# Performance work log

Hardware: AMD Instinct MI355X
Metric: run time of the kernel (lower is better)

Reference implementation:

```python
import jax, jax.numpy as jnp
import numpy as np

N_NODES = 100000
N_EDGES = 1600000
IN_DIM = 75
H_COMP = 64
H_BOND = 16
DEPTH = 3


def setup_inputs() -> dict:
    key = jax.random.key(0)
    ks = jax.random.split(key, 8)
    x = jax.random.normal(ks[0], (N_NODES, IN_DIM), dtype=jnp.float32)
    edge_index = jax.random.randint(ks[1], (2, N_EDGES), 0, N_NODES, dtype=jnp.int64)
    edge_attr = jax.random.normal(ks[2], (N_EDGES, H_BOND), dtype=jnp.float32)
    proj_w = jax.random.normal(ks[3], (IN_DIM, H_COMP), dtype=jnp.float32) * (1.0 / np.sqrt(IN_DIM))
    proj_b = jnp.zeros((H_COMP,), dtype=jnp.float32)
    u2_w = jax.random.normal(ks[4], (DEPTH, H_COMP + H_BOND, H_COMP), dtype=jnp.float32) * (1.0 / np.sqrt(H_COMP + H_BOND))
    u2_b = jnp.zeros((DEPTH, H_COMP), dtype=jnp.float32)
    u1_w = jax.random.normal(ks[5], (DEPTH, 2 * H_COMP, H_COMP), dtype=jnp.float32) * (1.0 / np.sqrt(2 * H_COMP))
    u1_b = jnp.zeros((DEPTH, H_COMP), dtype=jnp.float32)
    return {"x": x, "edge_index": edge_index, "edge_attr": edge_attr,
            "proj_w": proj_w, "proj_b": proj_b,
            "u2_w": u2_w, "u2_b": u2_b, "u1_w": u1_w, "u1_b": u1_b}


def reference(x, edge_index, edge_attr, proj_w, proj_b, u2_w, u2_b, u1_w, u1_b):
    # PyG default flow source_to_target: messages gathered from edge_index[0],
    # scatter-added at edge_index[1].
    src, dst = edge_index[0], edge_index[1]
    n = x.shape[0]
    # input projection: [N, in_dim] -> [N, H]
    h = x @ proj_w + proj_b
    for l in range(u2_w.shape[0]):
        # message: concat(x_j, edge_attr) -> Linear -> LeakyReLU(0.1)   [E, H+B] -> [E, H]
        z = jnp.concatenate([h[src], edge_attr], axis=-1)
        m = jax.nn.leaky_relu(z @ u2_w[l] + u2_b[l], negative_slope=0.1)
        # aggregate: scatter-add over destination nodes  [E, H] -> [N, H]
        agg = jax.ops.segment_sum(m, dst, num_segments=n)
        # update: concat(x, agg) -> Linear  [N, 2H] -> [N, H]
        h = jnp.concatenate([h, agg], axis=-1) @ u1_w[l] + u1_b[l]
    return h
```

## Files before the change

### kernel.cpp

```cpp
#include <hip/hip_runtime.h>

typedef __attribute__((ext_vector_type(8))) short frag_ab;
typedef __attribute__((ext_vector_type(4))) float frag_cd;
typedef __attribute__((ext_vector_type(4))) short short4v;

__device__ __forceinline__ short f2bf(float f) {
  union { float f; unsigned u; } v; v.f = f;
  unsigned r = v.u + 0x7fffu + ((v.u >> 16) & 1u);
  return (short)(r >> 16);
}

__global__ void wconv(const float* __restrict__ W, short* __restrict__ out,
                      int Keff, int S, int nmat)
{
  int tid = blockIdx.x * 256 + threadIdx.x;
  int per = S * 4 * 64;
  if (tid >= nmat * per) return;
  int m = tid / per, r = tid % per;
  int s = r / 256, ct = (r >> 6) & 3, ln = r & 63;
  const float* Wm = W + (size_t)m * Keff * 64;
  __align__(16) short tmp[8];
  for (int j = 0; j < 8; ++j) {
    int k = s * 32 + (ln >> 4) * 8 + j;
    int n = ct * 16 + (ln & 15);
    tmp[j] = (k < Keff) ? f2bf(Wm[k * 64 + n]) : (short)0;
  }
  *(uint4*)&out[((size_t)m * per + (size_t)(s * 4 + ct) * 64 + ln) * 8] = *(uint4*)tmp;
}

#define AS1 104
__global__ __launch_bounds__(256, 4) void proj_kernel(
    const float* __restrict__ x, const short* __restrict__ wt,
    const float* __restrict__ bias, short* __restrict__ hbf, int N)
{
  __shared__ __align__(16) short A[128 * AS1];
  int t = threadIdx.x;
  int nb = blockIdx.x * 128;
  int ln = t & 63;
  frag_ab bf[12];
  for (int s = 0; s < 3; ++s)
    for (int ct = 0; ct < 4; ++ct)
      bf[s * 4 + ct] = *(const frag_ab*)&wt[((size_t)(s * 4 + ct) * 64 + ln) * 8];
  for (int i = 0; i < 48; ++i) {
    int q = i * 256 + t; int el = q / 96; int c = q - el * 96;
    int rg = nb + el;
    float v = (c < 75 && rg < N) ? x[rg * 75 + c] : 0.f;
    A[el * AS1 + c] = f2bf(v);
  }
  __syncthreads();
  int wv = t >> 6;
  int lrow = ln & 15, lk = ln >> 4;
  frag_cd acc[2][4];
  for (int rt = 0; rt < 2; ++rt) for (int ct = 0; ct < 4; ++ct) {
    frag_cd z = {0.f, 0.f, 0.f, 0.f}; acc[rt][ct] = z;
  }
  for (int s = 0; s < 3; ++s) {
    frag_ab a0 = *(const frag_ab*)&A[(wv*32 + lrow) * AS1 + s*32 + lk*8];
    frag_ab a1 = *(const frag_ab*)&A[(wv*32 + 16 + lrow) * AS1 + s*32 + lk*8];
    for (int ct = 0; ct < 4; ++ct) {
      acc[0][ct] = __builtin_amdgcn_mfma_f32_16x16x32_bf16(a0, bf[s*4+ct], acc[0][ct], 0, 0, 0);
      acc[1][ct] = __builtin_amdgcn_mfma_f32_16x16x32_bf16(a1, bf[s*4+ct], acc[1][ct], 0, 0, 0);
    }
  }
  float bv[4];
  for (int ct = 0; ct < 4; ++ct) bv[ct] = bias[ct*16 + lrow];
  for (int rt = 0; rt < 2; ++rt)
    for (int ct = 0; ct < 4; ++ct)
      for (int r = 0; r < 4; ++r) {
        int row = wv*32 + rt*16 + lk*4 + r;
        int rg = nb + row;
        if (rg < N) hbf[(size_t)rg * 64 + ct*16 + lrow] = f2bf(acc[rt][ct][r] + bv[ct]);
      }
}

__global__ __launch_bounds__(256) void hist_kernel(
    const int* __restrict__ dst, int* __restrict__ counts, int E)
{
  int i = blockIdx.x * 256 + threadIdx.x;
  if (i < E) atomicAdd(&counts[dst[i]], 1);
}

#define SCAN_TILE 2048
__global__ __launch_bounds__(256) void scan_k1(
    const int* __restrict__ counts, int* __restrict__ offsets,
    int* __restrict__ bsum, int n)
{
  __shared__ int ts[256];
  int t = threadIdx.x;
  int base = blockIdx.x * SCAN_TILE + t * 8;
  int v[8]; int s = 0;
  for (int j = 0; j < 8; ++j) { v[j] = (base + j < n) ? counts[base + j] : 0; s += v[j]; }
  ts[t] = s; __syncthreads();
  for (int off = 1; off < 256; off <<= 1) {
    int x = (t >= off) ? ts[t - off] : 0;
    __syncthreads();
    ts[t] += x;
    __syncthreads();
  }
  if (t == 255) bsum[blockIdx.x] = ts[255];
  int run = (t > 0) ? ts[t - 1] : 0;
  for (int j = 0; j < 8; ++j) { if (base + j < n) offsets[base + j] = run; run += v[j]; }
}

__global__ void scan_k2(int* bsum, int nb) {
  if (threadIdx.x == 0 && blockIdx.x == 0) {
    int run = 0;
    for (int b = 0; b < nb; ++b) { int x = bsum[b]; bsum[b] = run; run += x; }
  }
}

__global__ __launch_bounds__(256) void scan_k3(
    int* __restrict__ offsets, const int* __restrict__ bsum, int n)
{
  int add = bsum[blockIdx.x];
  int base = blockIdx.x * SCAN_TILE + threadIdx.x;
  for (int j = 0; j < 8; ++j) { int i = base + j * 256; if (i < n) offsets[i] += add; }
}

__global__ __launch_bounds__(256) void scatter_kernel(
    const int* __restrict__ src, const int* __restrict__ dst,
    const float* __restrict__ attr, int* __restrict__ offsets,
    int2* __restrict__ sd, short* __restrict__ attr_s, int E)
{
  int e = blockIdx.x * 256 + threadIdx.x;
  if (e < E) {
    int d = dst[e];
    int p = atomicAdd(&offsets[d], 1);
    sd[p] = make_int2(src[e], d);
    const float4* a4 = (const float4*)(attr + (size_t)e * 16);
    float4 v0 = a4[0], v1 = a4[1], v2 = a4[2], v3 = a4[3];
    __align__(16) short tmp[16];
    tmp[0]=f2bf(v0.x); tmp[1]=f2bf(v0.y); tmp[2]=f2bf(v0.z); tmp[3]=f2bf(v0.w);
    tmp[4]=f2bf(v1.x); tmp[5]=f2bf(v1.y); tmp[6]=f2bf(v1.z); tmp[7]=f2bf(v1.w);
    tmp[8]=f2bf(v2.x); tmp[9]=f2bf(v2.y); tmp[10]=f2bf(v2.z); tmp[11]=f2bf(v2.w);
    tmp[12]=f2bf(v3.x); tmp[13]=f2bf(v3.y); tmp[14]=f2bf(v3.z); tmp[15]=f2bf(v3.w);
    *(uint4*)&attr_s[(size_t)p * 16]     = *(uint4*)&tmp[0];
    *(uint4*)&attr_s[(size_t)p * 16 + 8] = *(uint4*)&tmp[8];
  }
}

#define MS 66
__global__ __launch_bounds__(256, 4) void msg_kernel(
    const short* __restrict__ hbf, const short* __restrict__ attr_s,
    const int2* __restrict__ sd, const short* __restrict__ wt,
    const float* __restrict__ bias, float* __restrict__ agg, int E)
{
  __shared__ __align__(16) char u[128 * MS * 4];
  __shared__ int dstl[128];
  short* A = (short*)u;
  float* M = (float*)u;

  int t = threadIdx.x;
  int eb = blockIdx.x * 128;
  int ln = t & 63;

  if (t < 128) dstl[t] = (eb + t < E) ? sd[eb + t].y : -1;

  frag_ab bf[12];
  for (int s = 0; s < 3; ++s)
    for (int ct = 0; ct < 4; ++ct)
      bf[s * 4 + ct] = *(const frag_ab*)&wt[((size_t)(s * 4 + ct) * 64 + ln) * 8];

  for (int i = 0; i < 4; ++i) {
    int q = i * 256 + t; int el = q >> 3; int c = q & 7;
    int p = eb + el;
    int s = (p < E) ? sd[p].x : 0;
    *(uint4*)&A[el * AS1 + c * 8] = *(const uint4*)&hbf[(size_t)s * 64 + c * 8];
  }
  {
    int el = t >> 1, c = t & 1;
    int p = eb + el;
    uint4 v = {0u, 0u, 0u, 0u};
    if (p < E) v = *(const uint4*)&attr_s[(size_t)p * 16 + c * 8];
    *(uint4*)&A[el * AS1 + 64 + c * 8] = v;
    uint4 z = {0u, 0u, 0u, 0u};
    *(uint4*)&A[el * AS1 + 80 + c * 8] = z;
  }
  __syncthreads();

  int wv = t >> 6;
  int lrow = ln & 15, lk = ln >> 4;
  frag_cd acc[2][4];
  for (int rt = 0; rt < 2; ++rt) for (int ct = 0; ct < 4; ++ct) {
    frag_cd z = {0.f, 0.f, 0.f, 0.f}; acc[rt][ct] = z;
  }
  for (int s = 0; s < 3; ++s) {
    frag_ab a0 = *(const frag_ab*)&A[(wv*32 + lrow) * AS1 + s*32 + lk*8];
    frag_ab a1 = *(const frag_ab*)&A[(wv*32 + 16 + lrow) * AS1 + s*32 + lk*8];
    for (int ct = 0; ct < 4; ++ct) {
      acc[0][ct] = __builtin_amdgcn_mfma_f32_16x16x32_bf16(a0, bf[s*4+ct], acc[0][ct], 0, 0, 0);
      acc[1][ct] = __builtin_amdgcn_mfma_f32_16x16x32_bf16(a1, bf[s*4+ct], acc[1][ct], 0, 0, 0);
    }
  }
  float bv[4];
  for (int ct = 0; ct < 4; ++ct) bv[ct] = bias[ct*16 + lrow];

  __syncthreads();
  for (int rt = 0; rt < 2; ++rt)
    for (int ct = 0; ct < 4; ++ct)
      for (int r = 0; r < 4; ++r) {
        int row = wv*32 + rt*16 + lk*4 + r;
        float m = acc[rt][ct][r] + bv[ct];
        m = m > 0.f ? m : 0.1f * m;
        M[row * MS + ct*16 + lrow] = m;
      }
  __syncthreads();

  {
    int lo = wv * 32;
    bool end = false;
    if (ln < 32) {
      int di = dstl[lo + ln];
      end = (ln == 31) || (di != dstl[lo + ln + 1]);
    }
    unsigned long long bm = __ballot(end);
    unsigned em = (unsigned)bm;
    unsigned cm = em & ~(em & (0u - em)) & 0x7fffffffu;

    float s = 0.f;
#pragma unroll
    for (int i = 0; i < 32; ++i) {
      s += M[(lo + i) * MS + ln];
      if ((em >> i) & 1u) {
        int d = __builtin_amdgcn_readfirstlane(dstl[lo + i]);
        if (d >= 0) {
          float* dest = &agg[(size_t)d * 64 + ln];
          if ((cm >> i) & 1u) *dest = s;
          else unsafeAtomicAdd(dest, s);
        }
        s = 0.f;
      }
    }
  }
}

#define AS2 136
__global__ __launch_bounds__(256, 4) void upd_kernel(
    const short* __restrict__ hbf, float* __restrict__ agg,
    const short* __restrict__ wt, const float* __restrict__ bias,
    float* __restrict__ hout, short* __restrict__ hbfo, int N, int last)
{
  __shared__ __align__(16) short A[128 * AS2];
  int t = threadIdx.x;
  int nb = blockIdx.x * 128;
  int ln = t & 63;
  for (int i = 0; i < 4; ++i) {
    int q = i * 256 + t; int el = q >> 3; int c = q & 7;
    int rg = nb + el;
    uint4 v = {0u, 0u, 0u, 0u};
    if (rg < N) v = *(const uint4*)&hbf[(size_t)rg * 64 + c * 8];
    *(uint4*)&A[el * AS2 + c * 8] = v;
  }
  for (int i = 0; i < 8; ++i) {
    int q = i * 256 + t; int el = q >> 4; int c = q & 15;
    int rg = nb + el;
    float4 v = make_float4(0.f, 0.f, 0.f, 0.f);
    if (rg < N) {
      v = *(const float4*)&agg[(size_t)rg * 64 + c * 4];
      if (!last) {
        float4 z = make_float4(0.f, 0.f, 0.f, 0.f);
        *(float4*)&agg[(size_t)rg * 64 + c * 4] = z;
      }
    }
    short4v s4 = { f2bf(v.x), f2bf(v.y), f2bf(v.z), f2bf(v.w) };
    *(short4v*)&A[el * AS2 + 64 + c * 4] = s4;
  }
  __syncthreads();
  int wv = t >> 6;
  int lrow = ln & 15, lk = ln >> 4;
  frag_cd acc[2][4];
  for (int rt = 0; rt < 2; ++rt) for (int ct = 0; ct < 4; ++ct) {
    frag_cd z = {0.f, 0.f, 0.f, 0.f}; acc[rt][ct] = z;
  }
  for (int s = 0; s < 4; ++s) {
    frag_ab a0 = *(const frag_ab*)&A[(wv*32 + lrow) * AS2 + s*32 + lk*8];
    frag_ab a1 = *(const frag_ab*)&A[(wv*32 + 16 + lrow) * AS2 + s*32 + lk*8];
    for (int ct = 0; ct < 4; ++ct) {
      frag_ab b = *(const frag_ab*)&wt[((size_t)(s * 4 + ct) * 64 + ln) * 8];
      acc[0][ct] = __builtin_amdgcn_mfma_f32_16x16x32_bf16(a0, b, acc[0][ct], 0, 0, 0);
      acc[1][ct] = __builtin_amdgcn_mfma_f32_16x16x32_bf16(a1, b, acc[1][ct], 0, 0, 0);
    }
  }
  float bv[4];
  for (int ct = 0; ct < 4; ++ct) bv[ct] = bias[ct*16 + lrow];
  for (int rt = 0; rt < 2; ++rt)
    for (int ct = 0; ct < 4; ++ct)
      for (int r = 0; r < 4; ++r) {
        int row = wv*32 + rt*16 + lk*4 + r;
        int rg = nb + row;
        if (rg < N) {
          float v = acc[rt][ct][r] + bv[ct];
          if (last) hout[(size_t)rg * 64 + ct*16 + lrow] = v;
          hbfo[(size_t)rg * 64 + ct*16 + lrow] = f2bf(v);
        }
      }
}

extern "C" void kernel_launch(void* const* d_in, const int* in_sizes, int n_in,
                              void* d_out, int out_size, void* d_ws, size_t ws_size,
                              hipStream_t stream) {
  const float* x    = (const float*)d_in[0];
  const int*   ei   = (const int*)d_in[1];
  const float* attr = (const float*)d_in[2];
  const float* pw   = (const float*)d_in[3];
  const float* pb   = (const float*)d_in[4];
  const float* u2w  = (const float*)d_in[5];
  const float* u2b  = (const float*)d_in[6];
  const float* u1w  = (const float*)d_in[7];
  const float* u1b  = (const float*)d_in[8];

  const int N = in_sizes[0] / 75;
  const int E = in_sizes[1] / 2;
  const int* src = ei;
  const int* dst = ei + E;

  float* hout = (float*)d_out;
  char*  ws   = (char*)d_ws;
  size_t nh   = (size_t)N * 64;
  size_t off  = 0;
  short* hbf   = (short*)(ws + off); off += nh * 2;
  float* agg   = (float*)(ws + off); off += nh * 4;
  int2*  sd    = (int2*) (ws + off); off += (size_t)E * 8;
  short* attr_s= (short*)(ws + off); off += (size_t)E * 32;
  short* projt = (short*)(ws + off); off += 3 * 4 * 64 * 8 * 2;
  short* u2t   = (short*)(ws + off); off += (size_t)3 * 3 * 4 * 64 * 8 * 2;
  short* u1t   = (short*)(ws + off); off += (size_t)3 * 4 * 4 * 64 * 8 * 2;
  int* counts  = (int*)agg;
  int* offsets = counts + N;
  int* bsum    = offsets + N;

  const int NB = (N + 127) / 128;
  const int EB = (E + 127) / 128;
  const int GE = (E + 255) / 256;
  const int NS = (N + SCAN_TILE - 1) / SCAN_TILE;

  wconv<<<3, 256, 0, stream>>>(pw, projt, 75, 3, 1);
  wconv<<<9, 256, 0, stream>>>(u2w, u2t, 80, 3, 3);
  wconv<<<12, 256, 0, stream>>>(u1w, u1t, 128, 4, 3);
  proj_kernel<<<NB, 256, 0, stream>>>(x, projt, pb, hbf, N);
  hipMemsetAsync(counts, 0, (size_t)N * 4, stream);
  hist_kernel<<<GE, 256, 0, stream>>>(dst, counts, E);
  scan_k1<<<NS, 256, 0, stream>>>(counts, offsets, bsum, N);
  scan_k2<<<1, 64, 0, stream>>>(bsum, NS);
  scan_k3<<<NS, 256, 0, stream>>>(offsets, bsum, N);
  scatter_kernel<<<GE, 256, 0, stream>>>(src, dst, attr, offsets, sd, attr_s, E);

  hipMemsetAsync(agg, 0, nh * 4, stream);
  for (int l = 0; l < 3; ++l) {
    msg_kernel<<<EB, 256, 0, stream>>>(hbf, attr_s, sd,
                                       u2t + (size_t)l * 6144, u2b + l * 64,
                                       agg, E);
    upd_kernel<<<NB, 256, 0, stream>>>(hbf, agg,
                                       u1t + (size_t)l * 8192, u1b + l * 64,
                                       hout, hbf, N, l == 2);
  }
}
```

Baseline: 703.3 us.

## Load MFMA operands directly from global, drop LDS staging; precompute CSR ranks

The message and update kernels now load A-operand fragments straight from global memory into registers in MFMA layout instead of staging tiles through shared memory, which removes a barrier and LDS traffic. The message kernel also reloads weight fragments per step instead of keeping 12 in registers. The histogram kernel records each edge's rank so the scatter uses offset plus rank without a second atomic pass, and the block-sum scan becomes a wavefront shuffle scan. The trade-off is less coalesced global gathers (16-byte pieces per lane) and an extra per-edge rank array. The scan_k2 rewrite assumes at most 64 blocks.

New measurement: 695.9 us. Within noise of the previous version (-1.0%).

```diff
diff --git a/kernel.cpp b/kernel.cpp
--- a/kernel.cpp
+++ b/kernel.cpp
@@ -2,7 +2,6 @@
 
 typedef __attribute__((ext_vector_type(8))) short frag_ab;
 typedef __attribute__((ext_vector_type(4))) float frag_cd;
-typedef __attribute__((ext_vector_type(4))) short short4v;
 
 __device__ __forceinline__ short f2bf(float f) {
   union { float f; unsigned u; } v; v.f = f;
@@ -74,10 +73,11 @@
 }
 
 __global__ __launch_bounds__(256) void hist_kernel(
-    const int* __restrict__ dst, int* __restrict__ counts, int E)
+    const int* __restrict__ dst, int* __restrict__ counts,
+    int* __restrict__ rank, int E)
 {
   int i = blockIdx.x * 256 + threadIdx.x;
-  if (i < E) atomicAdd(&counts[dst[i]], 1);
+  if (i < E) rank[i] = atomicAdd(&counts[dst[i]], 1);
 }
 
 #define SCAN_TILE 2048
@@ -103,10 +103,14 @@
 }
 
 __global__ void scan_k2(int* bsum, int nb) {
-  if (threadIdx.x == 0 && blockIdx.x == 0) {
-    int run = 0;
-    for (int b = 0; b < nb; ++b) { int x = bsum[b]; bsum[b] = run; run += x; }
-  }
+  int ln = threadIdx.x;
+  int v = (ln < nb) ? bsum[ln] : 0;
+  int x = v;
+  for (int off = 1; off < 64; off <<= 1) {
+    int y = __shfl_up(x, off);
+    if (ln >= off) x += y;
+  }
+  if (ln < nb) bsum[ln] = x - v;
 }
 
 __global__ __launch_bounds__(256) void scan_k3(
@@ -119,13 +123,14 @@
 
 __global__ __launch_bounds__(256) void scatter_kernel(
     const int* __restrict__ src, const int* __restrict__ dst,
-    const float* __restrict__ attr, int* __restrict__ offsets,
-    int2* __restrict__ sd, short* __restrict__ attr_s, int E)
+    const float* __restrict__ attr, const int* __restrict__ offsets,
+    const int* __restrict__ rank, int2* __restrict__ sd,
+    short* __restrict__ attr_s, int E)
 {
   int e = blockIdx.x * 256 + threadIdx.x;
   if (e < E) {
     int d = dst[e];
-    int p = atomicAdd(&offsets[d], 1);
+    int p = offsets[d] + rank[e];
     sd[p] = make_int2(src[e], d);
     const float4* a4 = (const float4*)(attr + (size_t)e * 16);
     float4 v0 = a4[0], v1 = a4[1], v2 = a4[2], v3 = a4[3];
@@ -145,57 +150,42 @@
     const int2* __restrict__ sd, const short* __restrict__ wt,
     const float* __restrict__ bias, float* __restrict__ agg, int E)
 {
-  __shared__ __align__(16) char u[128 * MS * 4];
+  __shared__ float M[128 * MS];
   __shared__ int dstl[128];
-  short* A = (short*)u;
-  float* M = (float*)u;
-
   int t = threadIdx.x;
   int eb = blockIdx.x * 128;
   int ln = t & 63;
-
-  if (t < 128) dstl[t] = (eb + t < E) ? sd[eb + t].y : -1;
-
-  frag_ab bf[12];
-  for (int s = 0; s < 3; ++s)
-    for (int ct = 0; ct < 4; ++ct)
-      bf[s * 4 + ct] = *(const frag_ab*)&wt[((size_t)(s * 4 + ct) * 64 + ln) * 8];
-
-  for (int i = 0; i < 4; ++i) {
-    int q = i * 256 + t; int el = q >> 3; int c = q & 7;
-    int p = eb + el;
-    int s = (p < E) ? sd[p].x : 0;
-    *(uint4*)&A[el * AS1 + c * 8] = *(const uint4*)&hbf[(size_t)s * 64 + c * 8];
-  }
-  {
-    int el = t >> 1, c = t & 1;
-    int p = eb + el;
-    uint4 v = {0u, 0u, 0u, 0u};
-    if (p < E) v = *(const uint4*)&attr_s[(size_t)p * 16 + c * 8];
-    *(uint4*)&A[el * AS1 + 64 + c * 8] = v;
-    uint4 z = {0u, 0u, 0u, 0u};
-    *(uint4*)&A[el * AS1 + 80 + c * 8] = z;
-  }
-  __syncthreads();
-
   int wv = t >> 6;
   int lrow = ln & 15, lk = ln >> 4;
+
+  if (t < 128) dstl[t] = (eb + t < E) ? sd[eb + t].y : -1;
+
+  int p0 = eb + wv*32 + lrow;  if (p0 > E - 1) p0 = E - 1;
+  int p1 = p0 + 16;            if (p1 > E - 1) p1 = E - 1;
+  int s0 = sd[p0].x, s1 = sd[p1].x;
+
+  frag_ab a[3][2];
+  a[0][0] = *(const frag_ab*)&hbf[(size_t)s0 * 64 + lk*8];
+  a[0][1] = *(const frag_ab*)&hbf[(size_t)s1 * 64 + lk*8];
+  a[1][0] = *(const frag_ab*)&hbf[(size_t)s0 * 64 + 32 + lk*8];
+  a[1][1] = *(const frag_ab*)&hbf[(size_t)s1 * 64 + 32 + lk*8];
+  frag_ab z8 = {0,0,0,0,0,0,0,0};
+  a[2][0] = (lk < 2) ? *(const frag_ab*)&attr_s[(size_t)p0 * 16 + lk*8] : z8;
+  a[2][1] = (lk < 2) ? *(const frag_ab*)&attr_s[(size_t)p1 * 16 + lk*8] : z8;
+
   frag_cd acc[2][4];
   for (int rt = 0; rt < 2; ++rt) for (int ct = 0; ct < 4; ++ct) {
     frag_cd z = {0.f, 0.f, 0.f, 0.f}; acc[rt][ct] = z;
   }
-  for (int s = 0; s < 3; ++s) {
-    frag_ab a0 = *(const frag_ab*)&A[(wv*32 + lrow) * AS1 + s*32 + lk*8];
-    frag_ab a1 = *(const frag_ab*)&A[(wv*32 + 16 + lrow) * AS1 + s*32 + lk*8];
+  for (int s = 0; s < 3; ++s)
     for (int ct = 0; ct < 4; ++ct) {
-      acc[0][ct] = __builtin_amdgcn_mfma_f32_16x16x32_bf16(a0, bf[s*4+ct], acc[0][ct], 0, 0, 0);
-      acc[1][ct] = __builtin_amdgcn_mfma_f32_16x16x32_bf16(a1, bf[s*4+ct], acc[1][ct], 0, 0, 0);
-    }
-  }
+      frag_ab b = *(const frag_ab*)&wt[((size_t)(s * 4 + ct) * 64 + ln) * 8];
+      acc[0][ct] = __builtin_amdgcn_mfma_f32_16x16x32_bf16(a[s][0], b, acc[0][ct], 0, 0, 0);
+      acc[1][ct] = __builtin_amdgcn_mfma_f32_16x16x32_bf16(a[s][1], b, acc[1][ct], 0, 0, 0);
+    }
   float bv[4];
   for (int ct = 0; ct < 4; ++ct) bv[ct] = bias[ct*16 + lrow];
 
-  __syncthreads();
   for (int rt = 0; rt < 2; ++rt)
     for (int ct = 0; ct < 4; ++ct)
       for (int r = 0; r < 4; ++r) {
@@ -234,53 +224,55 @@
   }
 }
 
-#define AS2 136
 __global__ __launch_bounds__(256, 4) void upd_kernel(
     const short* __restrict__ hbf, float* __restrict__ agg,
     const short* __restrict__ wt, const float* __restrict__ bias,
     float* __restrict__ hout, short* __restrict__ hbfo, int N, int last)
 {
-  __shared__ __align__(16) short A[128 * AS2];
   int t = threadIdx.x;
   int nb = blockIdx.x * 128;
   int ln = t & 63;
-  for (int i = 0; i < 4; ++i) {
-    int q = i * 256 + t; int el = q >> 3; int c = q & 7;
-    int rg = nb + el;
-    uint4 v = {0u, 0u, 0u, 0u};
-    if (rg < N) v = *(const uint4*)&hbf[(size_t)rg * 64 + c * 8];
-    *(uint4*)&A[el * AS2 + c * 8] = v;
-  }
-  for (int i = 0; i < 8; ++i) {
-    int q = i * 256 + t; int el = q >> 4; int c = q & 15;
-    int rg = nb + el;
-    float4 v = make_float4(0.f, 0.f, 0.f, 0.f);
-    if (rg < N) {
-      v = *(const float4*)&agg[(size_t)rg * 64 + c * 4];
-      if (!last) {
-        float4 z = make_float4(0.f, 0.f, 0.f, 0.f);
-        *(float4*)&agg[(size_t)rg * 64 + c * 4] = z;
-      }
-    }
-    short4v s4 = { f2bf(v.x), f2bf(v.y), f2bf(v.z), f2bf(v.w) };
-    *(short4v*)&A[el * AS2 + 64 + c * 4] = s4;
-  }
-  __syncthreads();
   int wv = t >> 6;
   int lrow = ln & 15, lk = ln >> 4;
+  int r0 = nb + wv*32 + lrow;
+  int r1 = r0 + 16;
+
+  frag_ab z8 = {0,0,0,0,0,0,0,0};
+  frag_ab a[4][2];
+  a[0][0] = (r0 < N) ? *(const frag_ab*)&hbf[(size_t)r0 * 64 + lk*8]      : z8;
+  a[0][1] = (r1 < N) ? *(const frag_ab*)&hbf[(size_t)r1 * 64 + lk*8]      : z8;
+  a[1][0] = (r0 < N) ? *(const frag_ab*)&hbf[(size_t)r0 * 64 + 32 + lk*8] : z8;
+  a[1][1] = (r1 < N) ? *(const frag_ab*)&hbf[(size_t)r1 * 64 + 32 + lk*8] : z8;
+  for (int si = 0; si < 2; ++si) {
+    int cb = si * 32 + lk * 8;
+    for (int rt = 0; rt < 2; ++rt) {
+      int rg = rt ? r1 : r0;
+      frag_ab af = z8;
+      if (rg < N) {
+        float* ap = &agg[(size_t)rg * 64 + cb];
+        float4 v0 = *(const float4*)ap;
+        float4 v1 = *(const float4*)(ap + 4);
+        af[0]=f2bf(v0.x); af[1]=f2bf(v0.y); af[2]=f2bf(v0.z); af[3]=f2bf(v0.w);
+        af[4]=f2bf(v1.x); af[5]=f2bf(v1.y); af[6]=f2bf(v1.z); af[7]=f2bf(v1.w);
+        if (!last) {
+          float4 z = make_float4(0.f, 0.f, 0.f, 0.f);
+          *(float4*)ap = z; *(float4*)(ap + 4) = z;
+        }
+      }
+      a[2 + si][rt] = af;
+    }
+  }
+
   frag_cd acc[2][4];
   for (int rt = 0; rt < 2; ++rt) for (int ct = 0; ct < 4; ++ct) {
     frag_cd z = {0.f, 0.f, 0.f, 0.f}; acc[rt][ct] = z;
   }
-  for (int s = 0; s < 4; ++s) {
-    frag_ab a0 = *(const frag_ab*)&A[(wv*32 + lrow) * AS2 + s*32 + lk*8];
-    frag_ab a1 = *(const frag_ab*)&A[(wv*32 + 16 + lrow) * AS2 + s*32 + lk*8];
+  for (int s = 0; s < 4; ++s)
     for (int ct = 0; ct < 4; ++ct) {
       frag_ab b = *(const frag_ab*)&wt[((size_t)(s * 4 + ct) * 64 + ln) * 8];
-      acc[0][ct] = __builtin_amdgcn_mfma_f32_16x16x32_bf16(a0, b, acc[0][ct], 0, 0, 0);
-      acc[1][ct] = __builtin_amdgcn_mfma_f32_16x16x32_bf16(a1, b, acc[1][ct], 0, 0, 0);
-    }
-  }
+      acc[0][ct] = __builtin_amdgcn_mfma_f32_16x16x32_bf16(a[s][0], b, acc[0][ct], 0, 0, 0);
+      acc[1][ct] = __builtin_amdgcn_mfma_f32_16x16x32_bf16(a[s][1], b, acc[1][ct], 0, 0, 0);
+    }
   float bv[4];
   for (int ct = 0; ct < 4; ++ct) bv[ct] = bias[ct*16 + lrow];
   for (int rt = 0; rt < 2; ++rt)
@@ -322,6 +314,7 @@
   float* agg   = (float*)(ws + off); off += nh * 4;
   int2*  sd    = (int2*) (ws + off); off += (size_t)E * 8;
   short* attr_s= (short*)(ws + off); off += (size_t)E * 32;
+  int*   rank  = (int*)  (ws + off); off += (size_t)E * 4;
   short* projt = (short*)(ws + off); off += 3 * 4 * 64 * 8 * 2;
   short* u2t   = (short*)(ws + off); off += (size_t)3 * 3 * 4 * 64 * 8 * 2;
   short* u1t   = (short*)(ws + off); off += (size_t)3 * 4 * 4 * 64 * 8 * 2;
@@ -339,11 +332,12 @@
   wconv<<<12, 256, 0, stream>>>(u1w, u1t, 128, 4, 3);
   proj_kernel<<<NB, 256, 0, stream>>>(x, projt, pb, hbf, N);
   hipMemsetAsync(counts, 0, (size_t)N * 4, stream);
-  hist_kernel<<<GE, 256, 0, stream>>>(dst, counts, E);
+  hist_kernel<<<GE, 256, 0, stream>>>(dst, counts, rank, E);
   scan_k1<<<NS, 256, 0, stream>>>(counts, offsets, bsum, N);
   scan_k2<<<1, 64, 0, stream>>>(bsum, NS);
   scan_k3<<<NS, 256, 0, stream>>>(offsets, bsum, N);
-  scatter_kernel<<<GE, 256, 0, stream>>>(src, dst, attr, offsets, sd, attr_s, E);
+  scatter_kernel<<<GE, 256, 0, stream>>>(src, dst, attr, offsets, rank,
+                                         sd, attr_s, E);
 
   hipMemsetAsync(agg, 0, nh * 4, stream);
   for (int l = 0; l < 3; ++l) {
```
